# Kernel optimization log

Measured on AMD Instinct MI355X. Metric: run time of the kernel, lower is better.

## Reference

```python
import jax, jax.numpy as jnp
import numpy as np

IN_DIM = 128
OUT_DIM = 512
N_OBS = 25000
M_LANES = 400000
LANES_PER_OBS = M_LANES // N_OBS  # 16


def setup_inputs() -> dict:
    key = jax.random.key(0)
    k1, k2, k3, k4 = jax.random.split(key, 4)
    obs_encoding = jax.random.normal(k1, (N_OBS, IN_DIM), dtype=jnp.float32)
    lane_encoding = jax.random.normal(k2, (M_LANES, IN_DIM), dtype=jnp.float32)
    # Group ids: 16 lanes per obstacle, every group non-empty (matches the
    # implicit assumption of the torch loop, which would NaN on empty groups).
    same_obs_mask = (jnp.arange(M_LANES, dtype=jnp.int64) // LANES_PER_OBS).reshape(M_LANES, 1)
    # Linear(128 -> 512) params (torch default init style: uniform +-1/sqrt(fan_in))
    bound = 1.0 / np.sqrt(IN_DIM)
    W = jax.random.uniform(k3, (OUT_DIM, IN_DIM), minval=-bound, maxval=bound, dtype=jnp.float32)
    b = jax.random.uniform(k4, (OUT_DIM,), minval=-bound, maxval=bound, dtype=jnp.float32)
    return {"obs_encoding": obs_encoding, "lane_encoding": lane_encoding,
            "same_obs_mask": same_obs_mask, "W": W, "b": b}


def reference(obs_encoding, lane_encoding, same_obs_mask, W, b):
    N = obs_encoding.shape[0]
    seg = same_obs_mask[:, 0].astype(jnp.int32)          # [M]
    # encode = ReLU(Linear(lane_encoding)) : [M, OUT_DIM]
    enc = jax.nn.relu(jnp.einsum('mi,oi->mo', lane_encoding, W) + b)
    # per-group max pool
    maxp = jax.ops.segment_max(enc, seg, num_segments=N)  # [N, OUT_DIM]
    # per-group mean pool
    sums = jax.ops.segment_sum(enc, seg, num_segments=N)  # [N, OUT_DIM]
    cnt = jax.ops.segment_sum(jnp.ones((enc.shape[0],), dtype=enc.dtype), seg, num_segments=N)
    avgp = sums / cnt[:, None]
    return jnp.concatenate([maxp, avgp], axis=1)          # [N, 2*OUT_DIM]
```

## Files before the change

### kernel.cpp

```cpp
#include <hip/hip_runtime.h>
#include <hip/hip_bf16.h>


constexpr int IN_DIM  = 128;
constexpr int OUT_DIM = 512;
constexpr int N_OBS   = 25000;
constexpr int LPG     = 16;
constexpr int NBLK    = 512;

typedef short bf16x8 __attribute__((ext_vector_type(8)));
typedef float f32x4  __attribute__((ext_vector_type(4)));

static __device__ __forceinline__ short f2bf(float f) {
    union { __hip_bfloat16 h; short s; } u;
    u.h = __float2bfloat16(f);
    return u.s;
}

__global__ __launch_bounds__(256, 2)
void aggr_fused_kernel(const float* __restrict__ lane_enc,
                       const float* __restrict__ W,
                       const float* __restrict__ bias,
                       float* __restrict__ out) {
    __shared__ short stA[16][136];
    __shared__ float outL[2 * OUT_DIM];

    const int t    = threadIdx.x;
    const int lane = t & 63;
    const int wid  = t >> 6;
    const int lr   = lane & 15;
    const int lh   = lane >> 4;

    bf16x8 bfrag[8][4];
    float  bv[8];
#pragma unroll
    for (int tt = 0; tt < 8; ++tt) {
        const int col = wid * 128 + tt * 16 + lr;
        bv[tt] = bias[col];
#pragma unroll
        for (int kk = 0; kk < 4; ++kk) {
            const float4* wp = (const float4*)(W + (size_t)col * IN_DIM + kk * 32 + lh * 8);
            float4 w0 = wp[0], w1 = wp[1];
            bf16x8 bw;
            bw[0] = f2bf(w0.x); bw[1] = f2bf(w0.y); bw[2] = f2bf(w0.z); bw[3] = f2bf(w0.w);
            bw[4] = f2bf(w1.x); bw[5] = f2bf(w1.y); bw[6] = f2bf(w1.z); bw[7] = f2bf(w1.w);
            bfrag[tt][kk] = bw;
        }
    }

    const int srow = t >> 4;
    const int scol = (t & 15) * 8;

    float4 s0, s1;
    {
        const float4* p = (const float4*)(lane_enc + (size_t)blockIdx.x * (LPG * IN_DIM)) + t * 2;
        s0 = p[0]; s1 = p[1];
    }

    const float inv16 = 1.0f / 16.0f;

    for (int g = blockIdx.x; g < N_OBS; g += gridDim.x) {
        bf16x8 av;
        av[0] = f2bf(s0.x); av[1] = f2bf(s0.y); av[2] = f2bf(s0.z); av[3] = f2bf(s0.w);
        av[4] = f2bf(s1.x); av[5] = f2bf(s1.y); av[6] = f2bf(s1.z); av[7] = f2bf(s1.w);
        *(bf16x8*)&stA[srow][scol] = av;
        __syncthreads();

        bf16x8 af[4];
#pragma unroll
        for (int kk = 0; kk < 4; ++kk)
            af[kk] = *(const bf16x8*)&stA[lr][kk * 32 + lh * 8];

        const int gn = g + gridDim.x;
        if (gn < N_OBS) {
            const float4* p = (const float4*)(lane_enc + (size_t)gn * (LPG * IN_DIM)) + t * 2;
            s0 = p[0]; s1 = p[1];
        }

        f32x4 acc[8];
#pragma unroll
        for (int tt = 0; tt < 8; ++tt)
            acc[tt] = (f32x4){0.f, 0.f, 0.f, 0.f};
#pragma unroll
        for (int kk = 0; kk < 4; ++kk) {
#pragma unroll
            for (int tt = 0; tt < 8; ++tt)
                acc[tt] = __builtin_amdgcn_mfma_f32_16x16x32_bf16(af[kk], bfrag[tt][kk], acc[tt], 0, 0, 0);
        }

#pragma unroll
        for (int tt = 0; tt < 8; ++tt) {
            const float e0 = fmaxf(acc[tt][0] + bv[tt], 0.f);
            const float e1 = fmaxf(acc[tt][1] + bv[tt], 0.f);
            const float e2 = fmaxf(acc[tt][2] + bv[tt], 0.f);
            const float e3 = fmaxf(acc[tt][3] + bv[tt], 0.f);
            float mx = fmaxf(fmaxf(e0, e1), fmaxf(e2, e3));
            float sm = (e0 + e1) + (e2 + e3);
            mx = fmaxf(mx, __shfl_xor(mx, 16));
            mx = fmaxf(mx, __shfl_xor(mx, 32));
            sm += __shfl_xor(sm, 16);
            sm += __shfl_xor(sm, 32);
            if (lane < 16) {
                const int col = wid * 128 + tt * 16 + lane;
                outL[col]           = mx;
                outL[OUT_DIM + col] = sm;
            }
        }
        __syncthreads();

        float4 ov = *(const float4*)&outL[t * 4];
        if (t >= 128) { ov.x *= inv16; ov.y *= inv16; ov.z *= inv16; ov.w *= inv16; }
        *(float4*)(out + (size_t)g * (2 * OUT_DIM) + t * 4) = ov;
    }
}

extern "C" void kernel_launch(void* const* d_in, const int* in_sizes, int n_in,
                              void* d_out, int out_size, void* d_ws, size_t ws_size,
                              hipStream_t stream) {
    const float* lane_enc = (const float*)d_in[1];
    const float* W        = (const float*)d_in[3];
    const float* b        = (const float*)d_in[4];
    float* out            = (float*)d_out;

    aggr_fused_kernel<<<dim3(NBLK), dim3(256), 0, stream>>>(lane_enc, W, b, out);
}
```

Baseline: 103.2 us.

## Use 512-thread blocks with double-buffered swizzled LDS and direct output stores

Doubles the block to 512 threads so each wave holds 64 output features instead of 128, halving the register-resident weight fragments and allowing higher occupancy. The bf16 lane tile is double-buffered in LDS with an XOR swizzle, which cuts each group's iteration to one barrier and avoids bank conflicts. The output staging buffer is removed and lanes write max and mean values straight to global memory. In exchange, the direct output stores are narrower scalar writes, and each block now holds a full copy of the weights across twice as many threads.

Result: faster. 99.25 us (-3.8%).

```diff
diff --git a/kernel.cpp b/kernel.cpp
--- a/kernel.cpp
+++ b/kernel.cpp
@@ -5,10 +5,11 @@
 constexpr int IN_DIM  = 128;
 constexpr int OUT_DIM = 512;
 constexpr int N_OBS   = 25000;
-constexpr int LPG     = 16;
 constexpr int NBLK    = 512;
+constexpr int BLOCK   = 512;
 
 typedef short bf16x8 __attribute__((ext_vector_type(8)));
+typedef short bf16x4 __attribute__((ext_vector_type(4)));
 typedef float f32x4  __attribute__((ext_vector_type(4)));
 
 static __device__ __forceinline__ short f2bf(float f) {
@@ -17,29 +18,29 @@
     return u.s;
 }
 
-__global__ __launch_bounds__(256, 2)
+__global__ __launch_bounds__(BLOCK, 4)
 void aggr_fused_kernel(const float* __restrict__ lane_enc,
                        const float* __restrict__ W,
                        const float* __restrict__ bias,
                        float* __restrict__ out) {
-    __shared__ short stA[16][136];
-    __shared__ float outL[2 * OUT_DIM];
+    __shared__ char bufA[2][4096];
 
     const int t    = threadIdx.x;
     const int lane = t & 63;
     const int wid  = t >> 6;
-    const int lr   = lane & 15;
+    const int lc   = lane & 15;
     const int lh   = lane >> 4;
+    const int wfeat = wid * 64;
 
-    bf16x8 bfrag[8][4];
-    float  bv[8];
+    bf16x8 bfrag[4][4];
+    float  bv[4];
 #pragma unroll
-    for (int tt = 0; tt < 8; ++tt) {
-        const int col = wid * 128 + tt * 16 + lr;
-        bv[tt] = bias[col];
+    for (int tt = 0; tt < 4; ++tt) {
+        const int feat = wfeat + tt * 16 + lc;
+        bv[tt] = bias[feat];
 #pragma unroll
         for (int kk = 0; kk < 4; ++kk) {
-            const float4* wp = (const float4*)(W + (size_t)col * IN_DIM + kk * 32 + lh * 8);
+            const float4* wp = (const float4*)(W + (size_t)feat * IN_DIM + kk * 32 + lh * 8);
             float4 w0 = wp[0], w1 = wp[1];
             bf16x8 bw;
             bw[0] = f2bf(w0.x); bw[1] = f2bf(w0.y); bw[2] = f2bf(w0.z); bw[3] = f2bf(w0.w);
@@ -48,69 +49,66 @@
         }
     }
 
-    const int srow = t >> 4;
-    const int scol = (t & 15) * 8;
+    const int srow = t >> 5;
+    const int sq   = t & 31;
+    const int soff = (srow * 256 + sq * 8) ^ ((srow & 7) << 4);
 
-    float4 s0, s1;
+    int g = blockIdx.x;
+    float4 av = *(const float4*)(lane_enc + ((size_t)g * 16 + srow) * IN_DIM + sq * 4);
     {
-        const float4* p = (const float4*)(lane_enc + (size_t)blockIdx.x * (LPG * IN_DIM)) + t * 2;
-        s0 = p[0]; s1 = p[1];
+        bf16x4 b;
+        b[0] = f2bf(av.x); b[1] = f2bf(av.y); b[2] = f2bf(av.z); b[3] = f2bf(av.w);
+        *(bf16x4*)(&bufA[0][0] + soff) = b;
     }
+    __syncthreads();
 
     const float inv16 = 1.0f / 16.0f;
+    int cur = 0;
 
-    for (int g = blockIdx.x; g < N_OBS; g += gridDim.x) {
-        bf16x8 av;
-        av[0] = f2bf(s0.x); av[1] = f2bf(s0.y); av[2] = f2bf(s0.z); av[3] = f2bf(s0.w);
-        av[4] = f2bf(s1.x); av[5] = f2bf(s1.y); av[6] = f2bf(s1.z); av[7] = f2bf(s1.w);
-        *(bf16x8*)&stA[srow][scol] = av;
-        __syncthreads();
+    for (; g < N_OBS; g += NBLK) {
+        const int gn = g + NBLK;
+        if (gn < N_OBS)
+            av = *(const float4*)(lane_enc + ((size_t)gn * 16 + srow) * IN_DIM + sq * 4);
 
         bf16x8 af[4];
-#pragma unroll
-        for (int kk = 0; kk < 4; ++kk)
-            af[kk] = *(const bf16x8*)&stA[lr][kk * 32 + lh * 8];
-
-        const int gn = g + gridDim.x;
-        if (gn < N_OBS) {
-            const float4* p = (const float4*)(lane_enc + (size_t)gn * (LPG * IN_DIM)) + t * 2;
-            s0 = p[0]; s1 = p[1];
-        }
-
-        f32x4 acc[8];
-#pragma unroll
-        for (int tt = 0; tt < 8; ++tt)
-            acc[tt] = (f32x4){0.f, 0.f, 0.f, 0.f};
+        const char* rb = &bufA[cur][0];
 #pragma unroll
         for (int kk = 0; kk < 4; ++kk) {
-#pragma unroll
-            for (int tt = 0; tt < 8; ++tt)
-                acc[tt] = __builtin_amdgcn_mfma_f32_16x16x32_bf16(af[kk], bfrag[tt][kk], acc[tt], 0, 0, 0);
+            const int off = (lc * 256 + kk * 64 + lh * 16) ^ ((lc & 7) << 4);
+            af[kk] = *(const bf16x8*)(rb + off);
         }
 
 #pragma unroll
-        for (int tt = 0; tt < 8; ++tt) {
-            const float e0 = fmaxf(acc[tt][0] + bv[tt], 0.f);
-            const float e1 = fmaxf(acc[tt][1] + bv[tt], 0.f);
-            const float e2 = fmaxf(acc[tt][2] + bv[tt], 0.f);
-            const float e3 = fmaxf(acc[tt][3] + bv[tt], 0.f);
+        for (int tt = 0; tt < 4; ++tt) {
+            f32x4 acc = (f32x4){0.f, 0.f, 0.f, 0.f};
+#pragma unroll
+            for (int kk = 0; kk < 4; ++kk)
+                acc = __builtin_amdgcn_mfma_f32_16x16x32_bf16(af[kk], bfrag[tt][kk], acc, 0, 0, 0);
+
+            const float e0 = fmaxf(acc[0] + bv[tt], 0.f);
+            const float e1 = fmaxf(acc[1] + bv[tt], 0.f);
+            const float e2 = fmaxf(acc[2] + bv[tt], 0.f);
+            const float e3 = fmaxf(acc[3] + bv[tt], 0.f);
             float mx = fmaxf(fmaxf(e0, e1), fmaxf(e2, e3));
             float sm = (e0 + e1) + (e2 + e3);
             mx = fmaxf(mx, __shfl_xor(mx, 16));
             mx = fmaxf(mx, __shfl_xor(mx, 32));
             sm += __shfl_xor(sm, 16);
             sm += __shfl_xor(sm, 32);
-            if (lane < 16) {
-                const int col = wid * 128 + tt * 16 + lane;
-                outL[col]           = mx;
-                outL[OUT_DIM + col] = sm;
+
+            if (lane < 32) {
+                const float v = (lane < 16) ? mx : sm * inv16;
+                out[(size_t)g * (2 * OUT_DIM) + lh * OUT_DIM + wfeat + tt * 16 + lc] = v;
             }
         }
+
+        if (gn < N_OBS) {
+            bf16x4 b;
+            b[0] = f2bf(av.x); b[1] = f2bf(av.y); b[2] = f2bf(av.z); b[3] = f2bf(av.w);
+            *(bf16x4*)(&bufA[cur ^ 1][0] + soff) = b;
+        }
         __syncthreads();
-
-        float4 ov = *(const float4*)&outL[t * 4];
-        if (t >= 128) { ov.x *= inv16; ov.y *= inv16; ov.z *= inv16; ov.w *= inv16; }
-        *(float4*)(out + (size_t)g * (2 * OUT_DIM) + t * 4) = ov;
+        cur ^= 1;
     }
 }
 
@@ -122,5 +120,5 @@
     const float* b        = (const float*)d_in[4];
     float* out            = (float*)d_out;
 
-    aggr_fused_kernel<<<dim3(NBLK), dim3(256), 0, stream>>>(lane_enc, W, b, out);
+    aggr_fused_kernel<<<dim3(NBLK), dim3(BLOCK), 0, stream>>>(lane_enc, W, b, out);
 }
```
